# Kernel tuning notes

Hardware: AMD Instinct MI355X
Metric: run time of the kernel (lower is better)

Reference implementation:

```python
import jax, jax.numpy as jnp
import numpy as np

DT = 3600.0  # integration step [s], module-level constant in the source
N_STEPS = 1_048_576


def _build_abc(rc):
    """Build continuous-time LTI matrices of the 4R3C thermal network.

    rc[:4] -> resistances (Rg, Ri, Re, Rw), rc[4:] -> capacitances (Cai, Cwe, Cwi).
    Raw rc values are in (0,1); rescale to physically plausible ranges so that
    explicit Euler with dt=3600 s is stable (|dt * eig(A)| << 1).
    """
    Rg, Ri, Re, Rw = (rc[:4] * 10.0 + 1.0)          # K/W-ish
    Cai, Cwe, Cwi = (rc[4:] * 1e6 + 1e5)            # J/K-ish
    A = jnp.array([
        [-(1.0 / Rg + 1.0 / Ri) / Cai, 0.0, 1.0 / (Ri * Cai)],
        [0.0, -(1.0 / Re + 1.0 / Rw) / Cwe, 1.0 / (Rw * Cwe)],
        [1.0 / (Ri * Cwi), 1.0 / (Rw * Cwi), -(1.0 / Rw + 1.0 / Ri) / Cwi],
    ], dtype=rc.dtype)
    B = jnp.array([
        [1.0 / (Rg * Cai), 1.0 / Cai, 1.0 / Cai, 0.0, 0.0],
        [1.0 / (Re * Cwe), 0.0, 0.0, 1.0 / Cwe, 0.0],
        [0.0, 0.0, 0.0, 0.0, 1.0 / Cwi],
    ], dtype=rc.dtype)
    Cm = jnp.array([[1.0, 0.0, 0.0]], dtype=rc.dtype)  # y = Tai
    return A, B, Cm


def setup_inputs() -> dict:
    key = jax.random.key(0)
    k1, k2, k3 = jax.random.split(key, 3)
    x_init = jax.random.normal(k1, (3,), dtype=jnp.float32)
    u = jax.random.normal(k2, (N_STEPS, 5), dtype=jnp.float32)
    rc = jax.random.uniform(k3, (7,), dtype=jnp.float32)
    return {"x_init": x_init, "u": u, "rc": rc}


def reference(x_init, u, rc):
    A, B, Cm = _build_abc(rc)

    def step(x, ut):
        # model(xi, ui): rhs = A x + B u, y = C x  (y from pre-update state)
        dx = A @ x + B @ ut
        y = Cm @ x
        x_new = x + dx * DT  # explicit Euler
        return x_new, (x_new, y)

    _, (xsol, ysol) = jax.lax.scan(step, x_init, u)
    return xsol, ysol  # [T,3], [T,1]
```

## Files before the change

kernel.cpp:

```cpp
#include <hip/hip_runtime.h>

#define DTSTEP  3600.0
#define T_STEPS 1048576
#define LCH     16
#define NCH     (T_STEPS/LCH)
#define SUP     64
#define NSUP    (NCH/SUP)

#define OFF_M    0
#define OFF_N    9
#define OFF_PP   24
#define OFF_QP   78
#define OFF_FLAG 200
#define OFF_W    256
#define OFF_S    (OFF_W + NSUP*3)

__device__ inline float bf16up(unsigned short h){
  return __uint_as_float(((unsigned int)h) << 16);
}

__device__ inline void matsq3(double* C){
  double R[9];
#pragma unroll
  for (int r=0;r<3;r++){
#pragma unroll
    for (int c=0;c<3;c++){
      R[r*3+c] = C[r*3+0]*C[0+c] + C[r*3+1]*C[3+c] + C[r*3+2]*C[6+c];
    }
  }
#pragma unroll
  for (int k=0;k<9;k++) C[k]=R[k];
}

__global__ void k_setup(const void* __restrict__ rc_p, const void* __restrict__ u_p,
                        float* __restrict__ ws){
  if (threadIdx.x != 0 || blockIdx.x != 0) return;
  const unsigned short* up = (const unsigned short*)u_p;
  int cnt = 0;
  for (int k=0;k<32;k++){
    const float a = fabsf(bf16up(up[k]));
    if (!(a > 1e-4f && a < 100.0f)) cnt++;
  }
  const int isb = (cnt < 8);
  ws[OFF_FLAG] = isb ? 1.0f : 0.0f;
  float rcv[7];
  if (isb){
    const unsigned short* rp = (const unsigned short*)rc_p;
    for (int k=0;k<7;k++) rcv[k] = bf16up(rp[k]);
  } else {
    const float* rp = (const float*)rc_p;
    for (int k=0;k<7;k++) rcv[k] = rp[k];
  }
  const float Rg = rcv[0]*10.f+1.f, Ri = rcv[1]*10.f+1.f, Re = rcv[2]*10.f+1.f, Rw = rcv[3]*10.f+1.f;
  const float Cai = rcv[4]*1e6f+1e5f, Cwe = rcv[5]*1e6f+1e5f, Cwi = rcv[6]*1e6f+1e5f;
  double A[9];
  A[0] = -(1.0/Rg + 1.0/Ri)/Cai;          A[1] = 0.0;                              A[2] = 1.0/((double)Ri*(double)Cai);
  A[3] = 0.0;                              A[4] = -(1.0/Re + 1.0/Rw)/Cwe;          A[5] = 1.0/((double)Rw*(double)Cwe);
  A[6] = 1.0/((double)Ri*(double)Cwi);     A[7] = 1.0/((double)Rw*(double)Cwi);    A[8] = -(1.0/Rw + 1.0/Ri)/Cwi;
  double Bm[15] = {
    1.0/((double)Rg*(double)Cai), 1.0/(double)Cai, 1.0/(double)Cai, 0.0, 0.0,
    1.0/((double)Re*(double)Cwe), 0.0, 0.0, 1.0/(double)Cwe, 0.0,
    0.0, 0.0, 0.0, 0.0, 1.0/(double)Cwi };
  double Md[9];
#pragma unroll
  for (int k=0;k<9;k++) Md[k] = DTSTEP*A[k];
  Md[0]+=1.0; Md[4]+=1.0; Md[8]+=1.0;
#pragma unroll
  for (int k=0;k<9;k++)  ws[OFF_M+k] = (float)Md[k];
#pragma unroll
  for (int k=0;k<15;k++) ws[OFF_N+k] = (float)(DTSTEP*Bm[k]);
  double C[9];
#pragma unroll
  for (int k=0;k<9;k++) C[k]=Md[k];
  matsq3(C); matsq3(C); matsq3(C); matsq3(C);
  for (int r=0;r<6;r++){
    if (r) matsq3(C);
    for (int k=0;k<9;k++) ws[OFF_PP + r*9 + k] = (float)C[k];
  }
  matsq3(C);
  for (int r=0;r<10;r++){
    if (r) matsq3(C);
    for (int k=0;k<9;k++) ws[OFF_QP + r*9 + k] = (float)C[k];
  }
}

struct MN { float M0,M2,M4,M5,M6,M7,M8, N0,N1,N2,N5,N8,N14; };

__device__ inline MN load_mn(const float* __restrict__ ws){
  MN p;
  p.M0=ws[OFF_M+0]; p.M2=ws[OFF_M+2]; p.M4=ws[OFF_M+4]; p.M5=ws[OFF_M+5];
  p.M6=ws[OFF_M+6]; p.M7=ws[OFF_M+7]; p.M8=ws[OFF_M+8];
  p.N0=ws[OFF_N+0]; p.N1=ws[OFF_N+1]; p.N2=ws[OFF_N+2];
  p.N5=ws[OFF_N+5]; p.N8=ws[OFF_N+8]; p.N14=ws[OFF_N+14];
  return p;
}

__device__ inline void load_u(const void* __restrict__ u_p, int i, int isb, float* uu){
  if (isb){
    const uint4* p = reinterpret_cast<const uint4*>((const unsigned short*)u_p + (size_t)i*(LCH*5));
#pragma unroll
    for (int k=0;k<LCH*5/8;k++){
      const uint4 q = p[k];
      const unsigned int w[4] = {q.x,q.y,q.z,q.w};
#pragma unroll
      for (int m=0;m<4;m++){
        uu[k*8+2*m+0] = __uint_as_float((w[m] & 0xFFFFu) << 16);
        uu[k*8+2*m+1] = __uint_as_float(w[m] & 0xFFFF0000u);
      }
    }
  } else {
    const float4* u4 = reinterpret_cast<const float4*>((const float*)u_p) + (size_t)i*(LCH*5/4);
#pragma unroll
    for (int k=0;k<LCH*5/4;k++){
      const float4 q = u4[k];
      uu[k*4+0]=q.x; uu[k*4+1]=q.y; uu[k*4+2]=q.z; uu[k*4+3]=q.w;
    }
  }
}

__device__ inline void chunk_v(const float* uu, const MN& mn, float& v0, float& v1, float& v2){
  v0=0.f; v1=0.f; v2=0.f;
#pragma unroll
  for (int j=0;j<LCH;j++){
    const float u0=uu[j*5+0],u1=uu[j*5+1],u2=uu[j*5+2],u3=uu[j*5+3],u4v=uu[j*5+4];
    const float c0 = fmaf(mn.N0,u0, fmaf(mn.N1,u1, mn.N2*u2));
    const float c1 = fmaf(mn.N5,u0, mn.N8*u3);
    const float c2 = mn.N14*u4v;
    const float n0 = fmaf(mn.M0,v0, fmaf(mn.M2,v2, c0));
    const float n1 = fmaf(mn.M4,v1, fmaf(mn.M5,v2, c1));
    const float n2 = fmaf(mn.M6,v0, fmaf(mn.M7,v1, fmaf(mn.M8,v2, c2)));
    v0=n0; v1=n1; v2=n2;
  }
}

__global__ __launch_bounds__(256) void k_agg(const void* __restrict__ u,
                                             float* __restrict__ ws){
  __shared__ float buf[2][256*3];
  const int tid  = threadIdx.x;
  const int i    = blockIdx.x*256 + tid;
  const int lane = tid & 63;
  const int isb  = (ws[OFF_FLAG] != 0.0f);
  float uu[LCH*5];
  load_u(u, i, isb, uu);
  const MN mn = load_mn(ws);
  float t0,t1,t2;
  chunk_v(uu, mn, t0,t1,t2);
  buf[0][tid*3+0]=t0; buf[0][tid*3+1]=t1; buf[0][tid*3+2]=t2;
  __syncthreads();
  int cur=0;
#pragma unroll
  for (int r=0;r<6;r++){
    const int d = 1<<r;
    const float Q0=ws[OFF_PP+r*9+0],Q1=ws[OFF_PP+r*9+1],Q2=ws[OFF_PP+r*9+2],
                Q3=ws[OFF_PP+r*9+3],Q4=ws[OFF_PP+r*9+4],Q5=ws[OFF_PP+r*9+5],
                Q6=ws[OFF_PP+r*9+6],Q7=ws[OFF_PP+r*9+7],Q8=ws[OFF_PP+r*9+8];
    float p0=0.f,p1=0.f,p2=0.f;
    if (lane >= d){
      const int s=(tid-d)*3;
      p0=buf[cur][s+0]; p1=buf[cur][s+1]; p2=buf[cur][s+2];
    }
    t0 = fmaf(Q0,p0, fmaf(Q1,p1, fmaf(Q2,p2, t0)));
    t1 = fmaf(Q3,p0, fmaf(Q4,p1, fmaf(Q5,p2, t1)));
    t2 = fmaf(Q6,p0, fmaf(Q7,p1, fmaf(Q8,p2, t2)));
    buf[cur^1][tid*3+0]=t0; buf[cur^1][tid*3+1]=t1; buf[cur^1][tid*3+2]=t2;
    __syncthreads();
    cur ^= 1;
  }
  if (lane==63){
    const int sc = i>>6;
    ws[OFF_W+sc*3+0]=t0; ws[OFF_W+sc*3+1]=t1; ws[OFF_W+sc*3+2]=t2;
  }
}

__global__ __launch_bounds__(1024) void k_scan(const void* __restrict__ x_init_p,
                                               float* __restrict__ ws){
  __shared__ float buf[2][NSUP*3];
  const int t = threadIdx.x;
  float i0=ws[OFF_W+t*3+0], i1=ws[OFF_W+t*3+1], i2=ws[OFF_W+t*3+2];
  float xi0,xi1,xi2;
  if (ws[OFF_FLAG] != 0.0f){
    const unsigned short* xp = (const unsigned short*)x_init_p;
    xi0=bf16up(xp[0]); xi1=bf16up(xp[1]); xi2=bf16up(xp[2]);
  } else {
    const float* xp = (const float*)x_init_p;
    xi0=xp[0]; xi1=xp[1]; xi2=xp[2];
  }
  if (t==0){
    const float Q0=ws[OFF_QP+0],Q1=ws[OFF_QP+1],Q2=ws[OFF_QP+2],
                Q3=ws[OFF_QP+3],Q4=ws[OFF_QP+4],Q5=ws[OFF_QP+5],
                Q6=ws[OFF_QP+6],Q7=ws[OFF_QP+7],Q8=ws[OFF_QP+8];
    i0 = fmaf(Q0,xi0, fmaf(Q1,xi1, fmaf(Q2,xi2, i0)));
    i1 = fmaf(Q3,xi0, fmaf(Q4,xi1, fmaf(Q5,xi2, i1)));
    i2 = fmaf(Q6,xi0, fmaf(Q7,xi1, fmaf(Q8,xi2, i2)));
  }
  buf[0][t*3+0]=i0; buf[0][t*3+1]=i1; buf[0][t*3+2]=i2;
  __syncthreads();
  int cur=0;
#pragma unroll
  for (int r=0;r<10;r++){
    const int d = 1<<r;
    const float Q0=ws[OFF_QP+r*9+0],Q1=ws[OFF_QP+r*9+1],Q2=ws[OFF_QP+r*9+2],
                Q3=ws[OFF_QP+r*9+3],Q4=ws[OFF_QP+r*9+4],Q5=ws[OFF_QP+r*9+5],
                Q6=ws[OFF_QP+r*9+6],Q7=ws[OFF_QP+r*9+7],Q8=ws[OFF_QP+r*9+8];
    float p0=0.f,p1=0.f,p2=0.f;
    if (t >= d){
      const int s=(t-d)*3;
      p0=buf[cur][s+0]; p1=buf[cur][s+1]; p2=buf[cur][s+2];
    }
    i0 = fmaf(Q0,p0, fmaf(Q1,p1, fmaf(Q2,p2, i0)));
    i1 = fmaf(Q3,p0, fmaf(Q4,p1, fmaf(Q5,p2, i1)));
    i2 = fmaf(Q6,p0, fmaf(Q7,p1, fmaf(Q8,p2, i2)));
    buf[cur^1][t*3+0]=i0; buf[cur^1][t*3+1]=i1; buf[cur^1][t*3+2]=i2;
    __syncthreads();
    cur ^= 1;
  }
  if (t==0){ ws[OFF_S+0]=xi0; ws[OFF_S+1]=xi1; ws[OFF_S+2]=xi2; }
  if (t < NSUP-1){
    ws[OFF_S+(t+1)*3+0]=i0; ws[OFF_S+(t+1)*3+1]=i1; ws[OFF_S+(t+1)*3+2]=i2;
  }
}

__global__ __launch_bounds__(256) void k_expand(const void* __restrict__ u,
                                                float* __restrict__ ws,
                                                float* __restrict__ out){
  __shared__ float buf[2][256*3];
  const int tid  = threadIdx.x;
  const int i    = blockIdx.x*256 + tid;
  const int lane = tid & 63;
  const int sc   = i >> 6;
  const int isb  = (ws[OFF_FLAG] != 0.0f);
  float uu[LCH*5];
  load_u(u, i, isb, uu);
  const MN mn = load_mn(ws);
  float t0,t1,t2;
  chunk_v(uu, mn, t0,t1,t2);
  const float s0=ws[OFF_S+sc*3+0], s1=ws[OFF_S+sc*3+1], s2=ws[OFF_S+sc*3+2];
  if (lane==0){
    const float P0=ws[OFF_PP+0],P1=ws[OFF_PP+1],P2=ws[OFF_PP+2],
                P3=ws[OFF_PP+3],P4=ws[OFF_PP+4],P5=ws[OFF_PP+5],
                P6=ws[OFF_PP+6],P7=ws[OFF_PP+7],P8=ws[OFF_PP+8];
    const float a0 = fmaf(P0,s0, fmaf(P1,s1, fmaf(P2,s2, t0)));
    const float a1 = fmaf(P3,s0, fmaf(P4,s1, fmaf(P5,s2, t1)));
    const float a2 = fmaf(P6,s0, fmaf(P7,s1, fmaf(P8,s2, t2)));
    t0=a0; t1=a1; t2=a2;
  }
  buf[0][tid*3+0]=t0; buf[0][tid*3+1]=t1; buf[0][tid*3+2]=t2;
  __syncthreads();
  int cur=0;
#pragma unroll
  for (int r=0;r<6;r++){
    const int d = 1<<r;
    const float Q0=ws[OFF_PP+r*9+0],Q1=ws[OFF_PP+r*9+1],Q2=ws[OFF_PP+r*9+2],
                Q3=ws[OFF_PP+r*9+3],Q4=ws[OFF_PP+r*9+4],Q5=ws[OFF_PP+r*9+5],
                Q6=ws[OFF_PP+r*9+6],Q7=ws[OFF_PP+r*9+7],Q8=ws[OFF_PP+r*9+8];
    float p0=0.f,p1=0.f,p2=0.f;
    if (lane >= d){
      const int s=(tid-d)*3;
      p0=buf[cur][s+0]; p1=buf[cur][s+1]; p2=buf[cur][s+2];
    }
    t0 = fmaf(Q0,p0, fmaf(Q1,p1, fmaf(Q2,p2, t0)));
    t1 = fmaf(Q3,p0, fmaf(Q4,p1, fmaf(Q5,p2, t1)));
    t2 = fmaf(Q6,p0, fmaf(Q7,p1, fmaf(Q8,p2, t2)));
    buf[cur^1][tid*3+0]=t0; buf[cur^1][tid*3+1]=t1; buf[cur^1][tid*3+2]=t2;
    __syncthreads();
    cur ^= 1;
  }
  float x0,x1,x2;
  if (lane==0){ x0=s0; x1=s1; x2=s2; }
  else { const int s=(tid-1)*3; x0=buf[cur][s+0]; x1=buf[cur][s+1]; x2=buf[cur][s+2]; }

  float4* xo4 = reinterpret_cast<float4*>(out) + (size_t)i*12;
  float4* yo4 = reinterpret_cast<float4*>(out) + (size_t)(3*T_STEPS/4) + (size_t)i*4;
#pragma unroll
  for (int h=0; h<2; h++){
    float px[24]; float py[8];
#pragma unroll
    for (int j8=0;j8<8;j8++){
      const int j = h*8 + j8;
      py[j8]=x0;
      const float u0=uu[j*5+0],u1=uu[j*5+1],u2=uu[j*5+2],u3=uu[j*5+3],u4v=uu[j*5+4];
      const float c0 = fmaf(mn.N0,u0, fmaf(mn.N1,u1, mn.N2*u2));
      const float c1 = fmaf(mn.N5,u0, mn.N8*u3);
      const float c2 = mn.N14*u4v;
      const float n0 = fmaf(mn.M0,x0, fmaf(mn.M2,x2, c0));
      const float n1 = fmaf(mn.M4,x1, fmaf(mn.M5,x2, c1));
      const float n2 = fmaf(mn.M6,x0, fmaf(mn.M7,x1, fmaf(mn.M8,x2, c2)));
      x0=n0; x1=n1; x2=n2;
      px[j8*3+0]=x0; px[j8*3+1]=x1; px[j8*3+2]=x2;
    }
#pragma unroll
    for (int m=0;m<6;m++)
      xo4[h*6+m] = make_float4(px[4*m+0],px[4*m+1],px[4*m+2],px[4*m+3]);
#pragma unroll
    for (int m=0;m<2;m++)
      yo4[h*2+m] = make_float4(py[4*m+0],py[4*m+1],py[4*m+2],py[4*m+3]);
  }
}

extern "C" void kernel_launch(void* const* d_in, const int* in_sizes, int n_in,
                              void* d_out, int out_size, void* d_ws, size_t ws_size,
                              hipStream_t stream) {
  (void)out_size; (void)ws_size;
  const void* x_init = d_in[0];
  const void* u      = d_in[1];
  const void* rc     = d_in[2];
  for (int k=0;k<n_in;k++){
    if (in_sizes[k]==3) x_init = d_in[k];
    else if (in_sizes[k]==7) rc = d_in[k];
    else if (in_sizes[k]==T_STEPS*5) u = d_in[k];
  }
  float* ws = (float*)d_ws;
  float* out = (float*)d_out;

  k_setup <<<1, 64, 0, stream>>>(rc, u, ws);
  k_agg   <<<NCH/256, 256, 0, stream>>>(u, ws);
  k_scan  <<<1, NSUP, 0, stream>>>(x_init, ws);
  k_expand<<<NCH/256, 256, 0, stream>>>(u, ws, out);
}
```

Before: 32.69 us.

## Collapse four-kernel scan into two kernels with per-block setup and in-block carry scan

Removes the separate setup and single-block scan kernels. Each block now recomputes the matrix powers in shared memory, and the expand kernel redoes the 256-entry carry scan itself. Chunk length is halved to 8 and blocks grow to 512 threads, so each block covers 4096 steps and the intra-block scan takes 9 levels. The bf16 input detection path is dropped. This saves two launches and their serial dependencies, at the cost of redundant per-block setup in double precision on one thread and more barrier steps per block.

```diff
diff --git a/kernel.cpp b/kernel.cpp
--- a/kernel.cpp
+++ b/kernel.cpp
@@ -2,22 +2,11 @@
 
 #define DTSTEP  3600.0
 #define T_STEPS 1048576
-#define LCH     16
-#define NCH     (T_STEPS/LCH)
-#define SUP     64
-#define NSUP    (NCH/SUP)
-
-#define OFF_M    0
-#define OFF_N    9
-#define OFF_PP   24
-#define OFF_QP   78
-#define OFF_FLAG 200
-#define OFF_W    256
-#define OFF_S    (OFF_W + NSUP*3)
-
-__device__ inline float bf16up(unsigned short h){
-  return __uint_as_float(((unsigned int)h) << 16);
-}
+#define LCH     8
+#define TPB     512
+#define NBLK    256
+#define NAGG    NBLK
+
 
 __device__ inline void matsq3(double* C){
   double R[9];
@@ -32,90 +21,49 @@
   for (int k=0;k<9;k++) C[k]=R[k];
 }
 
-__global__ void k_setup(const void* __restrict__ rc_p, const void* __restrict__ u_p,
-                        float* __restrict__ ws){
-  if (threadIdx.x != 0 || blockIdx.x != 0) return;
-  const unsigned short* up = (const unsigned short*)u_p;
-  int cnt = 0;
-  for (int k=0;k<32;k++){
-    const float a = fabsf(bf16up(up[k]));
-    if (!(a > 1e-4f && a < 100.0f)) cnt++;
-  }
-  const int isb = (cnt < 8);
-  ws[OFF_FLAG] = isb ? 1.0f : 0.0f;
-  float rcv[7];
-  if (isb){
-    const unsigned short* rp = (const unsigned short*)rc_p;
-    for (int k=0;k<7;k++) rcv[k] = bf16up(rp[k]);
-  } else {
-    const float* rp = (const float*)rc_p;
-    for (int k=0;k<7;k++) rcv[k] = rp[k];
-  }
-  const float Rg = rcv[0]*10.f+1.f, Ri = rcv[1]*10.f+1.f, Re = rcv[2]*10.f+1.f, Rw = rcv[3]*10.f+1.f;
-  const float Cai = rcv[4]*1e6f+1e5f, Cwe = rcv[5]*1e6f+1e5f, Cwi = rcv[6]*1e6f+1e5f;
-  double A[9];
-  A[0] = -(1.0/Rg + 1.0/Ri)/Cai;          A[1] = 0.0;                              A[2] = 1.0/((double)Ri*(double)Cai);
-  A[3] = 0.0;                              A[4] = -(1.0/Re + 1.0/Rw)/Cwe;          A[5] = 1.0/((double)Rw*(double)Cwe);
-  A[6] = 1.0/((double)Ri*(double)Cwi);     A[7] = 1.0/((double)Rw*(double)Cwi);    A[8] = -(1.0/Rw + 1.0/Ri)/Cwi;
-  double Bm[15] = {
-    1.0/((double)Rg*(double)Cai), 1.0/(double)Cai, 1.0/(double)Cai, 0.0, 0.0,
-    1.0/((double)Re*(double)Cwe), 0.0, 0.0, 1.0/(double)Cwe, 0.0,
-    0.0, 0.0, 0.0, 0.0, 1.0/(double)Cwi };
+__device__ void setup_from_rc(const float* __restrict__ rc,
+                              float* __restrict__ sMN, float* __restrict__ sPW){
+  const float Rg = rc[0]*10.f+1.f, Ri = rc[1]*10.f+1.f, Re = rc[2]*10.f+1.f, Rw = rc[3]*10.f+1.f;
+  const float Cai = rc[4]*1e6f+1e5f, Cwe = rc[5]*1e6f+1e5f, Cwi = rc[6]*1e6f+1e5f;
   double Md[9];
-#pragma unroll
-  for (int k=0;k<9;k++) Md[k] = DTSTEP*A[k];
-  Md[0]+=1.0; Md[4]+=1.0; Md[8]+=1.0;
-#pragma unroll
-  for (int k=0;k<9;k++)  ws[OFF_M+k] = (float)Md[k];
-#pragma unroll
-  for (int k=0;k<15;k++) ws[OFF_N+k] = (float)(DTSTEP*Bm[k]);
+  Md[0] = 1.0 + DTSTEP*(-(1.0/Rg + 1.0/Ri)/Cai);
+  Md[1] = 0.0;
+  Md[2] = DTSTEP*(1.0/((double)Ri*(double)Cai));
+  Md[3] = 0.0;
+  Md[4] = 1.0 + DTSTEP*(-(1.0/Re + 1.0/Rw)/Cwe);
+  Md[5] = DTSTEP*(1.0/((double)Rw*(double)Cwe));
+  Md[6] = DTSTEP*(1.0/((double)Ri*(double)Cwi));
+  Md[7] = DTSTEP*(1.0/((double)Rw*(double)Cwi));
+  Md[8] = 1.0 + DTSTEP*(-(1.0/Rw + 1.0/Ri)/Cwi);
+  sMN[0]=(float)Md[0]; sMN[1]=(float)Md[2]; sMN[2]=(float)Md[4]; sMN[3]=(float)Md[5];
+  sMN[4]=(float)Md[6]; sMN[5]=(float)Md[7]; sMN[6]=(float)Md[8];
+  sMN[7] =(float)(DTSTEP*(1.0/((double)Rg*(double)Cai)));
+  sMN[8] =(float)(DTSTEP*(1.0/(double)Cai));
+  sMN[9] =(float)(DTSTEP*(1.0/(double)Cai));
+  sMN[10]=(float)(DTSTEP*(1.0/((double)Re*(double)Cwe)));
+  sMN[11]=(float)(DTSTEP*(1.0/(double)Cwe));
+  sMN[12]=(float)(DTSTEP*(1.0/(double)Cwi));
   double C[9];
 #pragma unroll
   for (int k=0;k<9;k++) C[k]=Md[k];
-  matsq3(C); matsq3(C); matsq3(C); matsq3(C);
-  for (int r=0;r<6;r++){
-    if (r) matsq3(C);
-    for (int k=0;k<9;k++) ws[OFF_PP + r*9 + k] = (float)C[k];
-  }
-  matsq3(C);
-  for (int r=0;r<10;r++){
-    if (r) matsq3(C);
-    for (int k=0;k<9;k++) ws[OFF_QP + r*9 + k] = (float)C[k];
+  for (int k=1;k<=19;k++){
+    matsq3(C);
+    if (k>=3){
+#pragma unroll
+      for (int j=0;j<9;j++) sPW[(k-3)*9+j] = (float)C[j];
+    }
   }
 }
 
 struct MN { float M0,M2,M4,M5,M6,M7,M8, N0,N1,N2,N5,N8,N14; };
 
-__device__ inline MN load_mn(const float* __restrict__ ws){
+__device__ inline MN mn_from_lds(const float* __restrict__ sMN){
   MN p;
-  p.M0=ws[OFF_M+0]; p.M2=ws[OFF_M+2]; p.M4=ws[OFF_M+4]; p.M5=ws[OFF_M+5];
-  p.M6=ws[OFF_M+6]; p.M7=ws[OFF_M+7]; p.M8=ws[OFF_M+8];
-  p.N0=ws[OFF_N+0]; p.N1=ws[OFF_N+1]; p.N2=ws[OFF_N+2];
-  p.N5=ws[OFF_N+5]; p.N8=ws[OFF_N+8]; p.N14=ws[OFF_N+14];
+  p.M0=sMN[0]; p.M2=sMN[1]; p.M4=sMN[2]; p.M5=sMN[3];
+  p.M6=sMN[4]; p.M7=sMN[5]; p.M8=sMN[6];
+  p.N0=sMN[7]; p.N1=sMN[8]; p.N2=sMN[9];
+  p.N5=sMN[10]; p.N8=sMN[11]; p.N14=sMN[12];
   return p;
-}
-
-__device__ inline void load_u(const void* __restrict__ u_p, int i, int isb, float* uu){
-  if (isb){
-    const uint4* p = reinterpret_cast<const uint4*>((const unsigned short*)u_p + (size_t)i*(LCH*5));
-#pragma unroll
-    for (int k=0;k<LCH*5/8;k++){
-      const uint4 q = p[k];
-      const unsigned int w[4] = {q.x,q.y,q.z,q.w};
-#pragma unroll
-      for (int m=0;m<4;m++){
-        uu[k*8+2*m+0] = __uint_as_float((w[m] & 0xFFFFu) << 16);
-        uu[k*8+2*m+1] = __uint_as_float(w[m] & 0xFFFF0000u);
-      }
-    }
-  } else {
-    const float4* u4 = reinterpret_cast<const float4*>((const float*)u_p) + (size_t)i*(LCH*5/4);
-#pragma unroll
-    for (int k=0;k<LCH*5/4;k++){
-      const float4 q = u4[k];
-      uu[k*4+0]=q.x; uu[k*4+1]=q.y; uu[k*4+2]=q.z; uu[k*4+3]=q.w;
-    }
-  }
 }
 
 __device__ inline void chunk_v(const float* uu, const MN& mn, float& v0, float& v1, float& v2){
@@ -133,29 +81,38 @@
   }
 }
 
-__global__ __launch_bounds__(256) void k_agg(const void* __restrict__ u,
+__global__ __launch_bounds__(TPB) void k_agg(const float* __restrict__ u,
+                                             const float* __restrict__ rc,
                                              float* __restrict__ ws){
-  __shared__ float buf[2][256*3];
-  const int tid  = threadIdx.x;
-  const int i    = blockIdx.x*256 + tid;
-  const int lane = tid & 63;
-  const int isb  = (ws[OFF_FLAG] != 0.0f);
+  __shared__ float sMN[13];
+  __shared__ float sPW[17*9];
+  __shared__ float buf[2][TPB*3];
+  const int tid = threadIdx.x;
+  const int blk = blockIdx.x;
+  const int i   = blk*TPB + tid;
   float uu[LCH*5];
-  load_u(u, i, isb, uu);
-  const MN mn = load_mn(ws);
+  const float4* u4 = reinterpret_cast<const float4*>(u) + (size_t)i*(LCH*5/4);
+#pragma unroll
+  for (int k=0;k<LCH*5/4;k++){
+    const float4 q = u4[k];
+    uu[k*4+0]=q.x; uu[k*4+1]=q.y; uu[k*4+2]=q.z; uu[k*4+3]=q.w;
+  }
+  if (tid==0) setup_from_rc(rc, sMN, sPW);
+  __syncthreads();
+  const MN mn = mn_from_lds(sMN);
   float t0,t1,t2;
   chunk_v(uu, mn, t0,t1,t2);
   buf[0][tid*3+0]=t0; buf[0][tid*3+1]=t1; buf[0][tid*3+2]=t2;
   __syncthreads();
   int cur=0;
 #pragma unroll
-  for (int r=0;r<6;r++){
+  for (int r=0;r<9;r++){
     const int d = 1<<r;
-    const float Q0=ws[OFF_PP+r*9+0],Q1=ws[OFF_PP+r*9+1],Q2=ws[OFF_PP+r*9+2],
-                Q3=ws[OFF_PP+r*9+3],Q4=ws[OFF_PP+r*9+4],Q5=ws[OFF_PP+r*9+5],
-                Q6=ws[OFF_PP+r*9+6],Q7=ws[OFF_PP+r*9+7],Q8=ws[OFF_PP+r*9+8];
+    const float Q0=sPW[r*9+0],Q1=sPW[r*9+1],Q2=sPW[r*9+2],
+                Q3=sPW[r*9+3],Q4=sPW[r*9+4],Q5=sPW[r*9+5],
+                Q6=sPW[r*9+6],Q7=sPW[r*9+7],Q8=sPW[r*9+8];
     float p0=0.f,p1=0.f,p2=0.f;
-    if (lane >= d){
+    if (tid >= d){
       const int s=(tid-d)*3;
       p0=buf[cur][s+0]; p1=buf[cur][s+1]; p2=buf[cur][s+2];
     }
@@ -166,95 +123,94 @@
     __syncthreads();
     cur ^= 1;
   }
-  if (lane==63){
-    const int sc = i>>6;
-    ws[OFF_W+sc*3+0]=t0; ws[OFF_W+sc*3+1]=t1; ws[OFF_W+sc*3+2]=t2;
-  }
-}
-
-__global__ __launch_bounds__(1024) void k_scan(const void* __restrict__ x_init_p,
-                                               float* __restrict__ ws){
-  __shared__ float buf[2][NSUP*3];
-  const int t = threadIdx.x;
-  float i0=ws[OFF_W+t*3+0], i1=ws[OFF_W+t*3+1], i2=ws[OFF_W+t*3+2];
-  float xi0,xi1,xi2;
-  if (ws[OFF_FLAG] != 0.0f){
-    const unsigned short* xp = (const unsigned short*)x_init_p;
-    xi0=bf16up(xp[0]); xi1=bf16up(xp[1]); xi2=bf16up(xp[2]);
-  } else {
-    const float* xp = (const float*)x_init_p;
-    xi0=xp[0]; xi1=xp[1]; xi2=xp[2];
-  }
-  if (t==0){
-    const float Q0=ws[OFF_QP+0],Q1=ws[OFF_QP+1],Q2=ws[OFF_QP+2],
-                Q3=ws[OFF_QP+3],Q4=ws[OFF_QP+4],Q5=ws[OFF_QP+5],
-                Q6=ws[OFF_QP+6],Q7=ws[OFF_QP+7],Q8=ws[OFF_QP+8];
-    i0 = fmaf(Q0,xi0, fmaf(Q1,xi1, fmaf(Q2,xi2, i0)));
-    i1 = fmaf(Q3,xi0, fmaf(Q4,xi1, fmaf(Q5,xi2, i1)));
-    i2 = fmaf(Q6,xi0, fmaf(Q7,xi1, fmaf(Q8,xi2, i2)));
-  }
-  buf[0][t*3+0]=i0; buf[0][t*3+1]=i1; buf[0][t*3+2]=i2;
+  if (tid==TPB-1){
+    ws[blk*3+0]=t0; ws[blk*3+1]=t1; ws[blk*3+2]=t2;
+  }
+}
+
+__global__ __launch_bounds__(TPB) void k_expand(const float* __restrict__ u,
+                                                const float* __restrict__ rc,
+                                                const float* __restrict__ x_init,
+                                                const float* __restrict__ ws,
+                                                float* __restrict__ out){
+  __shared__ float sMN[13];
+  __shared__ float sPW[17*9];
+  __shared__ float abuf[2][NAGG*3];
+  __shared__ float buf[2][TPB*3];
+  const int tid = threadIdx.x;
+  const int blk = blockIdx.x;
+  const int i   = blk*TPB + tid;
+  float uu[LCH*5];
+  const float4* u4 = reinterpret_cast<const float4*>(u) + (size_t)i*(LCH*5/4);
+#pragma unroll
+  for (int k=0;k<LCH*5/4;k++){
+    const float4 q = u4[k];
+    uu[k*4+0]=q.x; uu[k*4+1]=q.y; uu[k*4+2]=q.z; uu[k*4+3]=q.w;
+  }
+  if (tid==0) setup_from_rc(rc, sMN, sPW);
+  __syncthreads();
+  const float xi0=x_init[0], xi1=x_init[1], xi2=x_init[2];
+  float a0=0.f,a1=0.f,a2=0.f;
+  if (tid < NAGG){
+    a0=ws[tid*3+0]; a1=ws[tid*3+1]; a2=ws[tid*3+2];
+    if (tid==0){
+      const float R0=sPW[9*9+0],R1=sPW[9*9+1],R2=sPW[9*9+2],
+                  R3=sPW[9*9+3],R4=sPW[9*9+4],R5=sPW[9*9+5],
+                  R6=sPW[9*9+6],R7=sPW[9*9+7],R8=sPW[9*9+8];
+      a0 = fmaf(R0,xi0, fmaf(R1,xi1, fmaf(R2,xi2, a0)));
+      a1 = fmaf(R3,xi0, fmaf(R4,xi1, fmaf(R5,xi2, a1)));
+      a2 = fmaf(R6,xi0, fmaf(R7,xi1, fmaf(R8,xi2, a2)));
+    }
+    abuf[0][tid*3+0]=a0; abuf[0][tid*3+1]=a1; abuf[0][tid*3+2]=a2;
+  }
   __syncthreads();
   int cur=0;
 #pragma unroll
-  for (int r=0;r<10;r++){
+  for (int r=0;r<8;r++){
     const int d = 1<<r;
-    const float Q0=ws[OFF_QP+r*9+0],Q1=ws[OFF_QP+r*9+1],Q2=ws[OFF_QP+r*9+2],
-                Q3=ws[OFF_QP+r*9+3],Q4=ws[OFF_QP+r*9+4],Q5=ws[OFF_QP+r*9+5],
-                Q6=ws[OFF_QP+r*9+6],Q7=ws[OFF_QP+r*9+7],Q8=ws[OFF_QP+r*9+8];
+    const float Q0=sPW[(9+r)*9+0],Q1=sPW[(9+r)*9+1],Q2=sPW[(9+r)*9+2],
+                Q3=sPW[(9+r)*9+3],Q4=sPW[(9+r)*9+4],Q5=sPW[(9+r)*9+5],
+                Q6=sPW[(9+r)*9+6],Q7=sPW[(9+r)*9+7],Q8=sPW[(9+r)*9+8];
     float p0=0.f,p1=0.f,p2=0.f;
-    if (t >= d){
-      const int s=(t-d)*3;
-      p0=buf[cur][s+0]; p1=buf[cur][s+1]; p2=buf[cur][s+2];
-    }
-    i0 = fmaf(Q0,p0, fmaf(Q1,p1, fmaf(Q2,p2, i0)));
-    i1 = fmaf(Q3,p0, fmaf(Q4,p1, fmaf(Q5,p2, i1)));
-    i2 = fmaf(Q6,p0, fmaf(Q7,p1, fmaf(Q8,p2, i2)));
-    buf[cur^1][t*3+0]=i0; buf[cur^1][t*3+1]=i1; buf[cur^1][t*3+2]=i2;
+    if (tid < NAGG && tid >= d){
+      const int s=(tid-d)*3;
+      p0=abuf[cur][s+0]; p1=abuf[cur][s+1]; p2=abuf[cur][s+2];
+    }
+    if (tid < NAGG){
+      a0 = fmaf(Q0,p0, fmaf(Q1,p1, fmaf(Q2,p2, a0)));
+      a1 = fmaf(Q3,p0, fmaf(Q4,p1, fmaf(Q5,p2, a1)));
+      a2 = fmaf(Q6,p0, fmaf(Q7,p1, fmaf(Q8,p2, a2)));
+      abuf[cur^1][tid*3+0]=a0; abuf[cur^1][tid*3+1]=a1; abuf[cur^1][tid*3+2]=a2;
+    }
     __syncthreads();
     cur ^= 1;
   }
-  if (t==0){ ws[OFF_S+0]=xi0; ws[OFF_S+1]=xi1; ws[OFF_S+2]=xi2; }
-  if (t < NSUP-1){
-    ws[OFF_S+(t+1)*3+0]=i0; ws[OFF_S+(t+1)*3+1]=i1; ws[OFF_S+(t+1)*3+2]=i2;
-  }
-}
-
-__global__ __launch_bounds__(256) void k_expand(const void* __restrict__ u,
-                                                float* __restrict__ ws,
-                                                float* __restrict__ out){
-  __shared__ float buf[2][256*3];
-  const int tid  = threadIdx.x;
-  const int i    = blockIdx.x*256 + tid;
-  const int lane = tid & 63;
-  const int sc   = i >> 6;
-  const int isb  = (ws[OFF_FLAG] != 0.0f);
-  float uu[LCH*5];
-  load_u(u, i, isb, uu);
-  const MN mn = load_mn(ws);
+  float S0,S1,S2;
+  if (blk==0){ S0=xi0; S1=xi1; S2=xi2; }
+  else { const int s=(blk-1)*3; S0=abuf[cur][s+0]; S1=abuf[cur][s+1]; S2=abuf[cur][s+2]; }
+  const MN mn = mn_from_lds(sMN);
   float t0,t1,t2;
   chunk_v(uu, mn, t0,t1,t2);
-  const float s0=ws[OFF_S+sc*3+0], s1=ws[OFF_S+sc*3+1], s2=ws[OFF_S+sc*3+2];
-  if (lane==0){
-    const float P0=ws[OFF_PP+0],P1=ws[OFF_PP+1],P2=ws[OFF_PP+2],
-                P3=ws[OFF_PP+3],P4=ws[OFF_PP+4],P5=ws[OFF_PP+5],
-                P6=ws[OFF_PP+6],P7=ws[OFF_PP+7],P8=ws[OFF_PP+8];
-    const float a0 = fmaf(P0,s0, fmaf(P1,s1, fmaf(P2,s2, t0)));
-    const float a1 = fmaf(P3,s0, fmaf(P4,s1, fmaf(P5,s2, t1)));
-    const float a2 = fmaf(P6,s0, fmaf(P7,s1, fmaf(P8,s2, t2)));
-    t0=a0; t1=a1; t2=a2;
+  if (tid==0){
+    const float P0=sPW[0],P1=sPW[1],P2=sPW[2],
+                P3=sPW[3],P4=sPW[4],P5=sPW[5],
+                P6=sPW[6],P7=sPW[7],P8=sPW[8];
+    const float b0 = fmaf(P0,S0, fmaf(P1,S1, fmaf(P2,S2, t0)));
+    const float b1 = fmaf(P3,S0, fmaf(P4,S1, fmaf(P5,S2, t1)));
+    const float b2 = fmaf(P6,S0, fmaf(P7,S1, fmaf(P8,S2, t2)));
+    t0=b0; t1=b1; t2=b2;
   }
   buf[0][tid*3+0]=t0; buf[0][tid*3+1]=t1; buf[0][tid*3+2]=t2;
   __syncthreads();
-  int cur=0;
-#pragma unroll
-  for (int r=0;r<6;r++){
+  cur=0;
+#pragma unroll
+  for (int r=0;r<9;r++){
     const int d = 1<<r;
-    const float Q0=ws[OFF_PP+r*9+0],Q1=ws[OFF_PP+r*9+1],Q2=ws[OFF_PP+r*9+2],
-                Q3=ws[OFF_PP+r*9+3],Q4=ws[OFF_PP+r*9+4],Q5=ws[OFF_PP+r*9+5],
-                Q6=ws[OFF_PP+r*9+6],Q7=ws[OFF_PP+r*9+7],Q8=ws[OFF_PP+r*9+8];
+    const float Q0=sPW[r*9+0],Q1=sPW[r*9+1],Q2=sPW[r*9+2],
+                Q3=sPW[r*9+3],Q4=sPW[r*9+4],Q5=sPW[r*9+5],
+                Q6=sPW[r*9+6],Q7=sPW[r*9+7],Q8=sPW[r*9+8];
     float p0=0.f,p1=0.f,p2=0.f;
-    if (lane >= d){
+    if (tid >= d){
       const int s=(tid-d)*3;
       p0=buf[cur][s+0]; p1=buf[cur][s+1]; p2=buf[cur][s+2];
     }
@@ -266,54 +222,46 @@
     cur ^= 1;
   }
   float x0,x1,x2;
-  if (lane==0){ x0=s0; x1=s1; x2=s2; }
+  if (tid==0){ x0=S0; x1=S1; x2=S2; }
   else { const int s=(tid-1)*3; x0=buf[cur][s+0]; x1=buf[cur][s+1]; x2=buf[cur][s+2]; }
-
-  float4* xo4 = reinterpret_cast<float4*>(out) + (size_t)i*12;
-  float4* yo4 = reinterpret_cast<float4*>(out) + (size_t)(3*T_STEPS/4) + (size_t)i*4;
-#pragma unroll
-  for (int h=0; h<2; h++){
-    float px[24]; float py[8];
-#pragma unroll
-    for (int j8=0;j8<8;j8++){
-      const int j = h*8 + j8;
-      py[j8]=x0;
-      const float u0=uu[j*5+0],u1=uu[j*5+1],u2=uu[j*5+2],u3=uu[j*5+3],u4v=uu[j*5+4];
-      const float c0 = fmaf(mn.N0,u0, fmaf(mn.N1,u1, mn.N2*u2));
-      const float c1 = fmaf(mn.N5,u0, mn.N8*u3);
-      const float c2 = mn.N14*u4v;
-      const float n0 = fmaf(mn.M0,x0, fmaf(mn.M2,x2, c0));
-      const float n1 = fmaf(mn.M4,x1, fmaf(mn.M5,x2, c1));
-      const float n2 = fmaf(mn.M6,x0, fmaf(mn.M7,x1, fmaf(mn.M8,x2, c2)));
-      x0=n0; x1=n1; x2=n2;
-      px[j8*3+0]=x0; px[j8*3+1]=x1; px[j8*3+2]=x2;
-    }
-#pragma unroll
-    for (int m=0;m<6;m++)
-      xo4[h*6+m] = make_float4(px[4*m+0],px[4*m+1],px[4*m+2],px[4*m+3]);
-#pragma unroll
-    for (int m=0;m<2;m++)
-      yo4[h*2+m] = make_float4(py[4*m+0],py[4*m+1],py[4*m+2],py[4*m+3]);
-  }
+  float px[LCH*3], py[LCH];
+#pragma unroll
+  for (int j=0;j<LCH;j++){
+    py[j]=x0;
+    const float u0=uu[j*5+0],u1=uu[j*5+1],u2=uu[j*5+2],u3=uu[j*5+3],u4v=uu[j*5+4];
+    const float c0 = fmaf(mn.N0,u0, fmaf(mn.N1,u1, mn.N2*u2));
+    const float c1 = fmaf(mn.N5,u0, mn.N8*u3);
+    const float c2 = mn.N14*u4v;
+    const float n0 = fmaf(mn.M0,x0, fmaf(mn.M2,x2, c0));
+    const float n1 = fmaf(mn.M4,x1, fmaf(mn.M5,x2, c1));
+    const float n2 = fmaf(mn.M6,x0, fmaf(mn.M7,x1, fmaf(mn.M8,x2, c2)));
+    x0=n0; x1=n1; x2=n2;
+    px[j*3+0]=x0; px[j*3+1]=x1; px[j*3+2]=x2;
+  }
+  float4* xo4 = reinterpret_cast<float4*>(out) + (size_t)i*6;
+#pragma unroll
+  for (int m=0;m<6;m++)
+    xo4[m] = make_float4(px[4*m+0],px[4*m+1],px[4*m+2],px[4*m+3]);
+  float4* yo4 = reinterpret_cast<float4*>(out) + (size_t)(3*T_STEPS/4) + (size_t)i*2;
+  yo4[0] = make_float4(py[0],py[1],py[2],py[3]);
+  yo4[1] = make_float4(py[4],py[5],py[6],py[7]);
 }
 
 extern "C" void kernel_launch(void* const* d_in, const int* in_sizes, int n_in,
                               void* d_out, int out_size, void* d_ws, size_t ws_size,
                               hipStream_t stream) {
   (void)out_size; (void)ws_size;
-  const void* x_init = d_in[0];
-  const void* u      = d_in[1];
-  const void* rc     = d_in[2];
+  const float* x_init = (const float*)d_in[0];
+  const float* u      = (const float*)d_in[1];
+  const float* rc     = (const float*)d_in[2];
   for (int k=0;k<n_in;k++){
-    if (in_sizes[k]==3) x_init = d_in[k];
-    else if (in_sizes[k]==7) rc = d_in[k];
-    else if (in_sizes[k]==T_STEPS*5) u = d_in[k];
-  }
-  float* ws = (float*)d_ws;
+    if (in_sizes[k]==3) x_init = (const float*)d_in[k];
+    else if (in_sizes[k]==7) rc = (const float*)d_in[k];
+    else if (in_sizes[k]==T_STEPS*5) u = (const float*)d_in[k];
+  }
+  float* ws  = (float*)d_ws;
   float* out = (float*)d_out;
 
-  k_setup <<<1, 64, 0, stream>>>(rc, u, ws);
-  k_agg   <<<NCH/256, 256, 0, stream>>>(u, ws);
-  k_scan  <<<1, NSUP, 0, stream>>>(x_init, ws);
-  k_expand<<<NCH/256, 256, 0, stream>>>(u, ws, out);
-}
+  k_agg   <<<NBLK, TPB, 0, stream>>>(u, rc, ws);
+  k_expand<<<NBLK, TPB, 0, stream>>>(u, rc, x_init, ws, out);
+}
```

Measured after the change: 27.79 us. -15.0%, faster.
